# Kernel optimization log

Measured on AMD Instinct MI355X. Metric: run time of the kernel, lower is better.

The kernel has to match this reference:

```python
import jax, jax.numpy as jnp
import numpy as np

KA = 2  # kernel_att == stride

def _unfold2(t):
    # torch nn.Unfold(kernel=2, stride=2, pad=0): [B,C,H,W] -> [B, C, 4, L], L=(H/2)*(W/2)
    B, C, H, W = t.shape
    t = t.reshape(B, C, H // KA, KA, W // KA, KA).transpose(0, 1, 3, 5, 2, 4)
    return t.reshape(B, C, KA * KA, (H // KA) * (W // KA))

def _fold2(t, H, W):
    # inverse of _unfold2 (non-overlapping): [B, C, 4, L] -> [B, C, H, W]
    B, C, _, L = t.shape
    t = t.reshape(B, C, KA, KA, H // KA, W // KA).transpose(0, 1, 4, 2, 5, 3)
    return t.reshape(B, C, H, W)

def setup_inputs() -> dict:
    key = jax.random.key(0)
    ks = jax.random.split(key, 5)
    b, c, m, h, w = 4, 16, 8, 64, 64
    O = 64
    return {
        "x": jax.random.normal(ks[0], (b, c, m, h, w), jnp.float32),
        "w_q": jax.random.normal(ks[1], (O, m), jnp.float32) * 0.1,
        "w_k": jax.random.normal(ks[2], (O, m), jnp.float32) * 0.1,
        "w_v": jax.random.normal(ks[3], (O, m), jnp.float32) * 0.1,
        "w_p": jax.random.normal(ks[4], (2,), jnp.float32) * 0.1,
    }

def reference(x, w_q, w_k, w_v, w_p):
    b, c, m, h, w = x.shape
    O = w_q.shape[0]
    # res = AdaptiveAvgPool3d((1, dim, dim)) with h==w==dim -> mean over m only
    res = x.mean(axis=2, keepdims=True)            # [b, c, 1, h, w]
    xf = x.reshape(b * c, m, h, w)
    # 1x1 convs (bias-free) are channel matmuls
    q = jnp.einsum('om,bmhw->bohw', w_q, xf)       # [b*c, O, h, w]
    k = jnp.einsum('om,bmhw->bohw', w_k, xf)
    v = jnp.einsum('om,bmhw->bohw', w_v, xf)
    # relative position map pe = conv_p(position(h, w)) -> [1,1,h,w]
    loc_w = jnp.linspace(-1.0, 1.0, w)[None, :]    # varies along W
    loc_h = jnp.linspace(-1.0, 1.0, h)[:, None]    # varies along H
    pe = (w_p[0] * loc_w + w_p[1] * loc_h)[None, None]  # [1,1,h,w]
    q5 = q.reshape(b, c, O, h, w).transpose(0, 2, 1, 3, 4)  # permuted: [b, O, c, h, w]
    k5 = k.reshape(b, c, O, h, w) + pe             # pe broadcast over trailing (h,w)
    v5 = v.reshape(b, c, O, h, w)
    scaling = float(h) ** (-0.5)
    B = b * O
    q_att = (q5 * scaling).reshape(B, c, h, w)
    # NB: torch code views the UNpermuted [b,c,O,h,w] buffer as [b*O, c, h, w] (raw reinterpretation)
    k_att = k5.reshape(B, c, h, w)
    v_att = v5.reshape(B, c, h, w)
    uq = _unfold2(q_att)                           # [B, c, 4, L]
    uk = _unfold2(k_att) + _unfold2(pe)            # unfold_rpe broadcast: [B, c, 4, L]
    uv = _unfold2(v_att)
    # att[B,i,j,l] = sum_p q[B,i,p,l] * k[B,j,p,l]
    att = jnp.einsum('bipl,bjpl->bijl', uq, uk)    # [B, c, c, L]
    att = jax.nn.softmax(att, axis=2)
    out = jnp.einsum('bijl,bjpl->bipl', att, uv)   # [B, c, 4, L]
    out = _fold2(out, h, w)                        # [B, c, h, w]
    out = out.reshape(b, O, c, h, w).transpose(0, 2, 1, 3, 4)  # [b, c, O, h, w]
    return out + res
```

## Files before the change

### kernel.cpp

```cpp
#include <hip/hip_runtime.h>

typedef float v2f __attribute__((ext_vector_type(2)));


#if __has_builtin(__builtin_amdgcn_exp2f)
  #define EXP_FN(x) __builtin_amdgcn_exp2f(x)
  #define QSCALE 0.18033688011112043f
#else
  #define EXP_FN(x) __expf(x)
  #define QSCALE 0.125f
#endif
#if __has_builtin(__builtin_amdgcn_rcpf)
  #define RCP_FN(x) __builtin_amdgcn_rcpf(x)
#else
  #define RCP_FN(x) (1.0f/(x))
#endif

__global__ __launch_bounds__(512, 4) void adapt_attn(
    const float* __restrict__ x,  const float* __restrict__ wq,
    const float* __restrict__ wk, const float* __restrict__ wv,
    const float* __restrict__ wp, float* __restrict__ out)
{
    __shared__ __align__(16) v2f s_xk[2][2][8][2][16];
    __shared__ float4 s_uk[2][2][16][16];
    __shared__ float4 s_uv[2][2][16][16];

    const int tid = threadIdx.x;
    const int sub = tid >> 8;
    const int t8  = tid & 255;
    const int bid = blockIdx.x;
    const int u   = bid & 15;
    const int tg  = u * 2 + sub;
    const int o   = (bid >> 4) & 63;
    const int bb  = bid >> 10;
    const int r = o & 3, qch = o >> 2;

    const v2f*    __restrict__ x2 = (const v2f*)x;
    const float4* __restrict__ x4 = (const float4*)x;

    float4 s1;
    {
        const int f = t8 & 7, row = (t8 >> 3) & 1, m = (t8 >> 4) & 7, t = t8 >> 7;
        const int tile = tg * 2 + t;
        const int y0 = (tile >> 1) << 1, w8 = (tile & 1) * 8;
        s1 = x4[((bb * 16 + qch) * 8 + m) * 1024 + (y0 + row) * 16 + w8 + f];
    }

    const int p3 = t8 & 15, ig = (t8 >> 4) & 7, t3 = t8 >> 7;
    const int tile3 = tg * 2 + t3;
    const int y03 = (tile3 >> 1) << 1, ww03 = (tile3 & 1) << 4;
    const int sp = y03 * 32 + ww03 + p3;

    float wqr[8];
    #pragma unroll
    for (int m = 0; m < 8; m++)
        wqr[m] = QSCALE * wq[(o << 3) + m];

    v2f qa0[8], qb0[8], qa1[8], qb1[8];
    {
        const int bq0 = (bb * 16 + ig * 2) * 16384 + sp;
        const int bq1 = bq0 + 16384;
        #pragma unroll
        for (int m = 0; m < 8; m++) {
            qa0[m] = x2[bq0 + m * 2048];
            qb0[m] = x2[bq0 + m * 2048 + 32];
            qa1[m] = x2[bq1 + m * 2048];
            qb1[m] = x2[bq1 + m * 2048 + 32];
        }
    }

    v2f uqa0 = {0.f,0.f}, uqb0 = {0.f,0.f}, rsa0 = {0.f,0.f}, rsb0 = {0.f,0.f};
    v2f uqa1 = {0.f,0.f}, uqb1 = {0.f,0.f}, rsa1 = {0.f,0.f}, rsb1 = {0.f,0.f};
    #pragma unroll
    for (int m = 0; m < 8; m++) {
        uqa0 += qa0[m] * wqr[m];
        uqb0 += qb0[m] * wqr[m];
        rsa0 += qa0[m];
        rsb0 += qb0[m];
        uqa1 += qa1[m] * wqr[m];
        uqb1 += qb1[m] * wqr[m];
        rsa1 += qa1[m];
        rsb1 += qb1[m];
    }

    {
        const int f = t8 & 7, row = (t8 >> 3) & 1, m = (t8 >> 4) & 7, t = t8 >> 7;
        *(float4*)&s_xk[sub][t][m][row][f * 2] = s1;
    }

    const int p2 = t8 & 15, j2 = (t8 >> 4) & 15;
    float wkj[8], wvj[8];
    {
        const float4* wk4 = (const float4*)wk;
        const float4* wv4 = (const float4*)wv;
        const int rb = (r * 16 + j2) * 2;
        *(float4*)&wkj[0] = wk4[rb];   *(float4*)&wkj[4] = wk4[rb + 1];
        *(float4*)&wvj[0] = wv4[rb];   *(float4*)&wvj[4] = wv4[rb + 1];
    }
    const float wp0 = wp[0], wp1 = wp[1];
    __syncthreads();

    const float step = 2.0f / 63.0f;
    #pragma unroll
    for (int t = 0; t < 2; t++) {
        const int tile = tg * 2 + t;
        const int y0 = (tile >> 1) << 1, ww0 = (tile & 1) << 4;
        const int wwp = ww0 + p2;
        const float lx0 = -1.0f + step * (float)(wwp << 1);
        const float lx1 = lx0 + step;
        const float ly0 = -1.0f + step * (float)y0;
        const float ly1 = ly0 + step;
        v2f ka = { 2.0f * (wp0 * lx0 + wp1 * ly0), 2.0f * (wp0 * lx1 + wp1 * ly0) };
        v2f kb = { 2.0f * (wp0 * lx0 + wp1 * ly1), 2.0f * (wp0 * lx1 + wp1 * ly1) };
        v2f va = {0.f, 0.f}, vb = {0.f, 0.f};

        #pragma unroll
        for (int m = 0; m < 8; m++) {
            const v2f xa = s_xk[sub][t][m][0][p2];
            const v2f xb = s_xk[sub][t][m][1][p2];
            ka += xa * wkj[m]; kb += xb * wkj[m];
            va += xa * wvj[m]; vb += xb * wvj[m];
        }
        s_uk[sub][t][j2][p2] = make_float4(ka.x, ka.y, kb.x, kb.y);
        s_uv[sub][t][j2][p2] = make_float4(va.x, va.y, vb.x, vb.y);
    }
    __syncthreads();

    {
        v2f oa0 = {0.f, 0.f}, ob0 = {0.f, 0.f};
        v2f oa1 = {0.f, 0.f}, ob1 = {0.f, 0.f};
        float sum0 = 0.f, sum1 = 0.f;

        #pragma unroll
        for (int j = 0; j < 16; j++) {
            const float4 k4 = s_uk[sub][t3][j][p3];
            const float4 v4 = s_uv[sub][t3][j][p3];
            const v2f ka = {k4.x, k4.y}, kb = {k4.z, k4.w};
            const v2f va = {v4.x, v4.y}, vb = {v4.z, v4.w};

            v2f t0 = uqa0 * ka;
            t0 += uqb0 * kb;
            const float e0 = EXP_FN(t0.x + t0.y);
            sum0 += e0;
            oa0 += va * e0;
            ob0 += vb * e0;

            v2f t1 = uqa1 * ka;
            t1 += uqb1 * kb;
            const float e1 = EXP_FN(t1.x + t1.y);
            sum1 += e1;
            oa1 += va * e1;
            ob1 += vb * e1;
        }

        v2f* __restrict__ out2 = (v2f*)out;
        {
            const int i = ig * 2;
            const float rcp = RCP_FN(sum0);
            const v2f outa = oa0 * rcp + rsa0 * 0.125f;
            const v2f outb = ob0 * rcp + rsb0 * 0.125f;
            const int obi = ((bb * 16 + i) * 64 + o) * 2048 + sp;
            out2[obi]      = outa;
            out2[obi + 32] = outb;
        }
        {
            const int i = ig * 2 + 1;
            const float rcp = RCP_FN(sum1);
            const v2f outa = oa1 * rcp + rsa1 * 0.125f;
            const v2f outb = ob1 * rcp + rsb1 * 0.125f;
            const int obi = ((bb * 16 + i) * 64 + o) * 2048 + sp;
            out2[obi]      = outa;
            out2[obi + 32] = outb;
        }
    }
}

extern "C" void kernel_launch(void* const* d_in, const int* in_sizes, int n_in,
                              void* d_out, int out_size, void* d_ws, size_t ws_size,
                              hipStream_t stream) {
    const float* x  = (const float*)d_in[0];
    const float* wq = (const float*)d_in[1];
    const float* wk = (const float*)d_in[2];
    const float* wv = (const float*)d_in[3];
    const float* wp = (const float*)d_in[4];
    float* out = (float*)d_out;
    adapt_attn<<<dim3(4096), dim3(512), 0, stream>>>(x, wq, wk, wv, wp, out);
}
```

Before: 119.5 us.

## Halve block size and software-pipeline two tile groups per block

Each block now runs 256 threads instead of 512, and every thread processes the two tile groups one after the other instead of splitting them across two half-blocks. The work is interleaved so the q-projection loads for the second group overlap the k/v stage of the first, and the first group's softmax stage overlaps the second group's k/v compute, with both halves of the shared buffers used as double buffers. The aim is to hide global load latency through in-thread overlap and to make smaller blocks that are easier to schedule. In exchange each thread holds more live registers, which can lower occupancy, and there is an extra barrier per block.

```diff
diff --git a/kernel.cpp b/kernel.cpp
--- a/kernel.cpp
+++ b/kernel.cpp
@@ -16,7 +16,7 @@
   #define RCP_FN(x) (1.0f/(x))
 #endif
 
-__global__ __launch_bounds__(512, 4) void adapt_attn(
+__global__ __launch_bounds__(256, 4) void adapt_attn(
     const float* __restrict__ x,  const float* __restrict__ wq,
     const float* __restrict__ wk, const float* __restrict__ wv,
     const float* __restrict__ wp, float* __restrict__ out)
@@ -26,11 +26,8 @@
     __shared__ float4 s_uv[2][2][16][16];
 
     const int tid = threadIdx.x;
-    const int sub = tid >> 8;
-    const int t8  = tid & 255;
     const int bid = blockIdx.x;
     const int u   = bid & 15;
-    const int tg  = u * 2 + sub;
     const int o   = (bid >> 4) & 63;
     const int bb  = bid >> 10;
     const int r = o & 3, qch = o >> 2;
@@ -38,113 +35,98 @@
     const v2f*    __restrict__ x2 = (const v2f*)x;
     const float4* __restrict__ x4 = (const float4*)x;
 
-    float4 s1;
-    {
-        const int f = t8 & 7, row = (t8 >> 3) & 1, m = (t8 >> 4) & 7, t = t8 >> 7;
-        const int tile = tg * 2 + t;
-        const int y0 = (tile >> 1) << 1, w8 = (tile & 1) * 8;
-        s1 = x4[((bb * 16 + qch) * 8 + m) * 1024 + (y0 + row) * 16 + w8 + f];
+    const int sf = tid & 7, srow = (tid >> 3) & 1, sm = (tid >> 4) & 7, st = tid >> 7;
+    const int p2 = tid & 15, j2 = (tid >> 4) & 15;
+    const int p3 = tid & 15, ig = (tid >> 4) & 7, t3 = tid >> 7;
+    const float step = 2.0f / 63.0f;
+
+    const int kvbase = ((bb * 16 + qch) * 8 + sm) * 1024 + srow * 16 + sf;
+    float4 s1_0, s1_1;
+    {   const int tile0 = (2 * u + 0) * 2 + st;
+        s1_0 = x4[kvbase + ((tile0 >> 1) << 1) * 16 + (tile0 & 1) * 8];
+        const int tile1 = (2 * u + 1) * 2 + st;
+        s1_1 = x4[kvbase + ((tile1 >> 1) << 1) * 16 + (tile1 & 1) * 8];
     }
-
-    const int p3 = t8 & 15, ig = (t8 >> 4) & 7, t3 = t8 >> 7;
-    const int tile3 = tg * 2 + t3;
-    const int y03 = (tile3 >> 1) << 1, ww03 = (tile3 & 1) << 4;
-    const int sp = y03 * 32 + ww03 + p3;
-
-    float wqr[8];
-    #pragma unroll
-    for (int m = 0; m < 8; m++)
-        wqr[m] = QSCALE * wq[(o << 3) + m];
-
-    v2f qa0[8], qb0[8], qa1[8], qb1[8];
-    {
-        const int bq0 = (bb * 16 + ig * 2) * 16384 + sp;
-        const int bq1 = bq0 + 16384;
-        #pragma unroll
-        for (int m = 0; m < 8; m++) {
-            qa0[m] = x2[bq0 + m * 2048];
-            qb0[m] = x2[bq0 + m * 2048 + 32];
-            qa1[m] = x2[bq1 + m * 2048];
-            qb1[m] = x2[bq1 + m * 2048 + 32];
-        }
-    }
-
-    v2f uqa0 = {0.f,0.f}, uqb0 = {0.f,0.f}, rsa0 = {0.f,0.f}, rsb0 = {0.f,0.f};
-    v2f uqa1 = {0.f,0.f}, uqb1 = {0.f,0.f}, rsa1 = {0.f,0.f}, rsb1 = {0.f,0.f};
-    #pragma unroll
-    for (int m = 0; m < 8; m++) {
-        uqa0 += qa0[m] * wqr[m];
-        uqb0 += qb0[m] * wqr[m];
-        rsa0 += qa0[m];
-        rsb0 += qb0[m];
-        uqa1 += qa1[m] * wqr[m];
-        uqb1 += qb1[m] * wqr[m];
-        rsa1 += qa1[m];
-        rsb1 += qb1[m];
-    }
-
-    {
-        const int f = t8 & 7, row = (t8 >> 3) & 1, m = (t8 >> 4) & 7, t = t8 >> 7;
-        *(float4*)&s_xk[sub][t][m][row][f * 2] = s1;
-    }
-
-    const int p2 = t8 & 15, j2 = (t8 >> 4) & 15;
     float wkj[8], wvj[8];
-    {
-        const float4* wk4 = (const float4*)wk;
+    {   const float4* wk4 = (const float4*)wk;
         const float4* wv4 = (const float4*)wv;
         const int rb = (r * 16 + j2) * 2;
         *(float4*)&wkj[0] = wk4[rb];   *(float4*)&wkj[4] = wk4[rb + 1];
         *(float4*)&wvj[0] = wv4[rb];   *(float4*)&wvj[4] = wv4[rb + 1];
     }
+    float wqr[8];
+    #pragma unroll
+    for (int m = 0; m < 8; m++)
+        wqr[m] = QSCALE * wq[(o << 3) + m];
     const float wp0 = wp[0], wp1 = wp[1];
-    __syncthreads();
 
-    const float step = 2.0f / 63.0f;
-    #pragma unroll
-    for (int t = 0; t < 2; t++) {
-        const int tile = tg * 2 + t;
-        const int y0 = (tile >> 1) << 1, ww0 = (tile & 1) << 4;
-        const int wwp = ww0 + p2;
-        const float lx0 = -1.0f + step * (float)(wwp << 1);
-        const float lx1 = lx0 + step;
-        const float ly0 = -1.0f + step * (float)y0;
-        const float ly1 = ly0 + step;
-        v2f ka = { 2.0f * (wp0 * lx0 + wp1 * ly0), 2.0f * (wp0 * lx1 + wp1 * ly0) };
-        v2f kb = { 2.0f * (wp0 * lx0 + wp1 * ly1), 2.0f * (wp0 * lx1 + wp1 * ly1) };
-        v2f va = {0.f, 0.f}, vb = {0.f, 0.f};
+    auto qconv = [&](int tgi, v2f& uqa0, v2f& uqb0, v2f& uqa1, v2f& uqb1,
+                     v2f& rsa0, v2f& rsb0, v2f& rsa1, v2f& rsb1) -> int {
+        const int tile3 = tgi * 2 + t3;
+        const int y03 = (tile3 >> 1) << 1, ww03 = (tile3 & 1) << 4;
+        const int sp = y03 * 32 + ww03 + p3;
+        const int bq0 = (bb * 16 + ig * 2) * 16384 + sp;
+        const int bq1 = bq0 + 16384;
+        #pragma unroll
+        for (int mh = 0; mh < 4; mh++) {
+            const int m0 = 2 * mh, m1 = 2 * mh + 1;
+            const v2f a0  = x2[bq0 + m0 * 2048],      a0b = x2[bq0 + m0 * 2048 + 32];
+            const v2f a1  = x2[bq0 + m1 * 2048],      a1b = x2[bq0 + m1 * 2048 + 32];
+            const v2f c0  = x2[bq1 + m0 * 2048],      c0b = x2[bq1 + m0 * 2048 + 32];
+            const v2f c1  = x2[bq1 + m1 * 2048],      c1b = x2[bq1 + m1 * 2048 + 32];
+            uqa0 += a0 * wqr[m0];  uqa0 += a1 * wqr[m1];
+            uqb0 += a0b * wqr[m0]; uqb0 += a1b * wqr[m1];
+            uqa1 += c0 * wqr[m0];  uqa1 += c1 * wqr[m1];
+            uqb1 += c0b * wqr[m0]; uqb1 += c1b * wqr[m1];
+            rsa0 += a0;  rsa0 += a1;   rsb0 += a0b; rsb0 += a1b;
+            rsa1 += c0;  rsa1 += c1;   rsb1 += c0b; rsb1 += c1b;
+        }
+        return sp;
+    };
 
+    auto stage2 = [&](int tgi, int pb) {
         #pragma unroll
-        for (int m = 0; m < 8; m++) {
-            const v2f xa = s_xk[sub][t][m][0][p2];
-            const v2f xb = s_xk[sub][t][m][1][p2];
-            ka += xa * wkj[m]; kb += xb * wkj[m];
-            va += xa * wvj[m]; vb += xb * wvj[m];
+        for (int t = 0; t < 2; t++) {
+            const int tile = tgi * 2 + t;
+            const int y0 = (tile >> 1) << 1, ww0 = (tile & 1) << 4;
+            const int wwp = ww0 + p2;
+            const float lx0 = -1.0f + step * (float)(wwp << 1);
+            const float lx1 = lx0 + step;
+            const float ly0 = -1.0f + step * (float)y0;
+            const float ly1 = ly0 + step;
+            v2f ka = { 2.0f * (wp0 * lx0 + wp1 * ly0), 2.0f * (wp0 * lx1 + wp1 * ly0) };
+            v2f kb = { 2.0f * (wp0 * lx0 + wp1 * ly1), 2.0f * (wp0 * lx1 + wp1 * ly1) };
+            v2f va = {0.f, 0.f}, vb = {0.f, 0.f};
+            #pragma unroll
+            for (int m = 0; m < 8; m++) {
+                const v2f xa = s_xk[pb][t][m][0][p2];
+                const v2f xb = s_xk[pb][t][m][1][p2];
+                ka += xa * wkj[m]; kb += xb * wkj[m];
+                va += xa * wvj[m]; vb += xb * wvj[m];
+            }
+            s_uk[pb][t][j2][p2] = make_float4(ka.x, ka.y, kb.x, kb.y);
+            s_uv[pb][t][j2][p2] = make_float4(va.x, va.y, vb.x, vb.y);
         }
-        s_uk[sub][t][j2][p2] = make_float4(ka.x, ka.y, kb.x, kb.y);
-        s_uv[sub][t][j2][p2] = make_float4(va.x, va.y, vb.x, vb.y);
-    }
-    __syncthreads();
+    };
 
-    {
+    auto stage3 = [&](int pb, int sp,
+                      v2f uqa0, v2f uqb0, v2f uqa1, v2f uqb1,
+                      v2f rsa0, v2f rsb0, v2f rsa1, v2f rsb1) {
         v2f oa0 = {0.f, 0.f}, ob0 = {0.f, 0.f};
         v2f oa1 = {0.f, 0.f}, ob1 = {0.f, 0.f};
         float sum0 = 0.f, sum1 = 0.f;
-
         #pragma unroll
         for (int j = 0; j < 16; j++) {
-            const float4 k4 = s_uk[sub][t3][j][p3];
-            const float4 v4 = s_uv[sub][t3][j][p3];
+            const float4 k4 = s_uk[pb][t3][j][p3];
+            const float4 v4 = s_uv[pb][t3][j][p3];
             const v2f ka = {k4.x, k4.y}, kb = {k4.z, k4.w};
             const v2f va = {v4.x, v4.y}, vb = {v4.z, v4.w};
-
             v2f t0 = uqa0 * ka;
             t0 += uqb0 * kb;
             const float e0 = EXP_FN(t0.x + t0.y);
             sum0 += e0;
             oa0 += va * e0;
             ob0 += vb * e0;
-
             v2f t1 = uqa1 * ka;
             t1 += uqb1 * kb;
             const float e1 = EXP_FN(t1.x + t1.y);
@@ -152,10 +134,8 @@
             oa1 += va * e1;
             ob1 += vb * e1;
         }
-
         v2f* __restrict__ out2 = (v2f*)out;
-        {
-            const int i = ig * 2;
+        {   const int i = ig * 2;
             const float rcp = RCP_FN(sum0);
             const v2f outa = oa0 * rcp + rsa0 * 0.125f;
             const v2f outb = ob0 * rcp + rsb0 * 0.125f;
@@ -163,8 +143,7 @@
             out2[obi]      = outa;
             out2[obi + 32] = outb;
         }
-        {
-            const int i = ig * 2 + 1;
+        {   const int i = ig * 2 + 1;
             const float rcp = RCP_FN(sum1);
             const v2f outa = oa1 * rcp + rsa1 * 0.125f;
             const v2f outb = ob1 * rcp + rsb1 * 0.125f;
@@ -172,7 +151,30 @@
             out2[obi]      = outa;
             out2[obi + 32] = outb;
         }
-    }
+    };
+
+    v2f uqa0_0={0.f,0.f}, uqb0_0={0.f,0.f}, uqa1_0={0.f,0.f}, uqb1_0={0.f,0.f};
+    v2f rsa0_0={0.f,0.f}, rsb0_0={0.f,0.f}, rsa1_0={0.f,0.f}, rsb1_0={0.f,0.f};
+    const int sp0 = qconv(2 * u + 0, uqa0_0, uqb0_0, uqa1_0, uqb1_0,
+                          rsa0_0, rsb0_0, rsa1_0, rsb1_0);
+    *(float4*)&s_xk[0][st][sm][srow][sf * 2] = s1_0;
+    __syncthreads();
+
+    stage2(2 * u + 0, 0);
+    v2f uqa0_1={0.f,0.f}, uqb0_1={0.f,0.f}, uqa1_1={0.f,0.f}, uqb1_1={0.f,0.f};
+    v2f rsa0_1={0.f,0.f}, rsb0_1={0.f,0.f}, rsa1_1={0.f,0.f}, rsb1_1={0.f,0.f};
+    const int sp1 = qconv(2 * u + 1, uqa0_1, uqb0_1, uqa1_1, uqb1_1,
+                          rsa0_1, rsb0_1, rsa1_1, rsb1_1);
+    *(float4*)&s_xk[1][st][sm][srow][sf * 2] = s1_1;
+    __syncthreads();
+
+    stage3(0, sp0, uqa0_0, uqb0_0, uqa1_0, uqb1_0,
+           rsa0_0, rsb0_0, rsa1_0, rsb1_0);
+    stage2(2 * u + 1, 1);
+    __syncthreads();
+
+    stage3(1, sp1, uqa0_1, uqb0_1, uqa1_1, uqb1_1,
+           rsa0_1, rsb0_1, rsa1_1, rsb1_1);
 }
 
 extern "C" void kernel_launch(void* const* d_in, const int* in_sizes, int n_in,
@@ -184,5 +186,5 @@
     const float* wv = (const float*)d_in[3];
     const float* wp = (const float*)d_in[4];
     float* out = (float*)d_out;
-    adapt_attn<<<dim3(4096), dim3(512), 0, stream>>>(x, wq, wk, wv, wp, out);
+    adapt_attn<<<dim3(4096), dim3(256), 0, stream>>>(x, wq, wk, wv, wp, out);
 }
```

Measured after the change: 119.3 us. About the same (-0.2%).
